# Kernel tuning notes

Measured on AMD Instinct MI355X. Metric: run time of the kernel, lower is better.

## Reference

```python
import jax, jax.numpy as jnp
import numpy as np

N_CH = 64
EPS = 1e-5


def _lhat():
    # adj=None branch: dist = ones - eye; adj_dist = exp(-dist/std) (torch.std is unbiased).
    dist = np.ones((N_CH, N_CH), np.float32) - np.eye(N_CH, dtype=np.float32)
    std = dist.std(ddof=1)
    A = np.exp(-dist / std).astype(np.float32)  # all entries > threshold=1e-4 -> fully connected w/ self loops
    deg = A.sum(axis=1)
    dinv = 1.0 / np.sqrt(deg)
    L = np.eye(N_CH, dtype=np.float32) - dinv[:, None] * A * dinv[None, :]  # sym-normalized Laplacian
    # ChebConv rescaling: Lhat = 2L/lambda_max - I with lambda_max=2 -> L - I
    return jnp.asarray(L - np.eye(N_CH, dtype=np.float32))


def _cheb(x, Lhat, W):
    # x: (B, N, Fin), W: (K, Fin, Fout). Chebyshev recursion, bias=False.
    Tx0 = x
    out = jnp.einsum('bnf,fo->bno', Tx0, W[0])
    Tx1 = jnp.einsum('nm,bmf->bnf', Lhat, Tx0)
    out = out + jnp.einsum('bnf,fo->bno', Tx1, W[1])
    for k in range(2, W.shape[0]):
        Tx2 = 2.0 * jnp.einsum('nm,bmf->bnf', Lhat, Tx1) - Tx0
        out = out + jnp.einsum('bnf,fo->bno', Tx2, W[k])
        Tx0, Tx1 = Tx1, Tx2
    return out


def _bn(x, g, b):
    # PyG BatchNorm (training mode): stats over all nodes in the batch -> axes (0,1).
    mu = jnp.mean(x, axis=(0, 1), keepdims=True)
    var = jnp.mean((x - mu) ** 2, axis=(0, 1), keepdims=True)
    return g * (x - mu) * jax.lax.rsqrt(var + EPS) + b


def setup_inputs() -> dict:
    key = jax.random.key(0)
    ks = jax.random.split(key, 4)
    B, F_IN, D = 4096, 256, 128
    x = jax.random.normal(ks[0], (B, N_CH, F_IN), dtype=jnp.float32)
    W1 = jax.random.normal(ks[1], (5, F_IN, D), dtype=jnp.float32) * 0.05
    W2 = jax.random.normal(ks[2], (3, D, D), dtype=jnp.float32) * 0.08
    W3 = jax.random.normal(ks[3], (3, D, D), dtype=jnp.float32) * 0.08
    ones = jnp.ones((D,), jnp.float32)
    zeros = jnp.zeros((D,), jnp.float32)
    return {'x': x, 'W1': W1, 'W2': W2, 'W3': W3,
            'g1': ones, 'b1': zeros, 'g2': ones, 'b2': zeros, 'g3': ones, 'b3': zeros}


def reference(x, W1, W2, W3, g1, b1, g2, b2, g3, b3):
    Lhat = _lhat()
    h = jax.nn.relu(_bn(_cheb(x, Lhat, W1), g1, b1))
    h = jax.nn.relu(_bn(_cheb(h, Lhat, W2), g2, b2))
    h = jax.nn.relu(_bn(_cheb(h, Lhat, W3), g3, b3))
    # global_mean_pool over nodes of each graph (dropout p=0 is identity)
    return jnp.mean(h, axis=1)  # (B, embed_dim)
```

## Files before the change

### kernel.cpp

```cpp
#include <hip/hip_runtime.h>
#include <cmath>


typedef __attribute__((ext_vector_type(8))) short bf16x8;
typedef __attribute__((ext_vector_type(4))) float f32x4;

typedef __attribute__((address_space(1))) const unsigned int guint_t;
typedef __attribute__((address_space(3))) unsigned int luint_t;

constexpr int BATCH = 4096;
constexpr int DCH   = 128;
constexpr float INV_NROWS = 1.0f / 262144.0f;

constexpr size_t OFF_G1   = 0;
constexpr size_t OFF_G2   = 32768;
constexpr size_t OFF_G3   = 49152;
constexpr size_t OFF_RAW  = 65536;
constexpr size_t OFF_Y    = 1180416;

struct Coeffs { float a[5]; float b[5]; };

__device__ __forceinline__ unsigned short f2bf(float f) {
  unsigned u = __float_as_uint(f);
  u += 0x7FFFu + ((u >> 16) & 1u);
  return (unsigned short)(u >> 16);
}
__device__ __forceinline__ float bf2f(unsigned short s) {
  return __uint_as_float(((unsigned)s) << 16);
}

__global__ __launch_bounds__(256) void prep_gran(const float* __restrict__ W1,
                                                 const float* __restrict__ W2,
                                                 const float* __restrict__ W3,
                                                 float* __restrict__ ws,
                                                 float* __restrict__ raw, Coeffs co)
{
  int id = blockIdx.x * 256 + threadIdx.x;
  if (id < 6144) raw[id] = 0.f;
  const float* W; int CIN, K, r; const float* cf; unsigned short* dst;
  if (id < 8192) {
    W = W1; CIN = 256; K = 5; r = id & 4095;
    cf = (id >= 4096) ? co.b : co.a;
    dst = (unsigned short*)(ws + OFF_G1) + (size_t)id * 8;
  } else if (id < 12288) {
    int e = id - 8192; W = W2; CIN = 128; K = 3; r = e & 2047;
    cf = (e >= 2048) ? co.b : co.a;
    dst = (unsigned short*)(ws + OFF_G2) + (size_t)e * 8;
  } else {
    int e = id - 12288; W = W3; CIN = 128; K = 3; r = e & 2047;
    cf = (e >= 2048) ? co.b : co.a;
    dst = (unsigned short*)(ws + OFF_G3) + (size_t)e * 8;
  }
  int kt  = r >> 9;
  int ct  = (r >> 6) & 7;
  int ln  = r & 63;
  int col = ct * 16 + (ln & 15);
  int f0  = kt * 32 + (ln >> 4) * 8;
  bf16x8 g;
#pragma unroll
  for (int i = 0; i < 8; ++i) {
    float s = 0.f;
    for (int k = 0; k < K; ++k)
      s = fmaf(cf[k], W[((size_t)k * CIN + f0 + i) * DCH + col], s);
    g[i] = (short)f2bf(s);
  }
  *reinterpret_cast<bf16x8*>(dst) = g;
}

template <int CIN, bool FIRST>
__global__ __launch_bounds__(512) void layer_k(
    const float* __restrict__ inF,
    const unsigned short* __restrict__ inB,
    unsigned short* __restrict__ yout,
    const unsigned short* __restrict__ gran,
    const float* __restrict__ rawIn,
    const float* __restrict__ gam, const float* __restrict__ bet,
    float* __restrict__ rawOut)
{
  constexpr int NKT = CIN / 32;
  constexpr int NG  = CIN * 16;

  __shared__ unsigned short sB[CIN * 256];
  __shared__ unsigned short slab[8][1152];
  __shared__ float sJw[4][2][DCH];
  __shared__ float sScale[DCH];
  __shared__ float sShift[DCH];

  const int tid = threadIdx.x;
  const int wv  = tid >> 6;
  const int p   = wv >> 1;
  const int h   = wv & 1;
  const int l   = tid & 63;
  const int lr  = l & 15;
  const int lk  = l >> 4;

  {
    const char* gB = reinterpret_cast<const char*>(gran);
    char* lB = reinterpret_cast<char*>(&sB[0]);
#pragma unroll
    for (int i = 0; i < (CIN * 512) / 8192; ++i) {
      const int c = i * 8 + wv;
      __builtin_amdgcn_global_load_lds(
          (guint_t*)(gB + (size_t)c * 1024 + (size_t)l * 16),
          (luint_t*)(lB + c * 1024), 16, 0, 0);
    }
  }
  if constexpr (!FIRST) {
    if (tid < DCH) {
      float ss = 0.f, qq = 0.f;
#pragma unroll
      for (int s = 0; s < 8; ++s) {
        ss += rawIn[s * 256 + tid];
        qq += rawIn[s * 256 + 128 + tid];
      }
      float mu  = ss * INV_NROWS;
      float var = qq * INV_NROWS - mu * mu;
      float rs  = rsqrtf(var + 1e-5f);
      float sc  = gam[tid] * rs;
      sScale[tid] = sc;
      sShift[tid] = fmaf(-mu, sc, bet[tid]);
    }
  }
  __syncthreads();

  const bf16x8* sBu = reinterpret_cast<const bf16x8*>(&sB[0]);

  float psum[8], psq[8];
#pragma unroll
  for (int ct = 0; ct < 8; ++ct) { psum[ct] = 0.f; psq[ct] = 0.f; }

#pragma unroll 1
  for (int it = 0; it < 4; ++it) {
    const int batch = blockIdx.x * 16 + it * 4 + p;

    f32x4 acc[8][2];
    f32x4 accJ[8];
#pragma unroll
    for (int ct = 0; ct < 8; ++ct) {
#pragma unroll
      for (int mt = 0; mt < 2; ++mt)
#pragma unroll
        for (int r = 0; r < 4; ++r) acc[ct][mt][r] = 0.f;
#pragma unroll
      for (int r = 0; r < 4; ++r) accJ[ct][r] = 0.f;
    }

#pragma unroll
    for (int kt = 0; kt < NKT; ++kt) {
      bf16x8 af[2];
      float vs[8];
#pragma unroll
      for (int i = 0; i < 8; ++i) vs[i] = 0.f;

      if constexpr (FIRST) {
        const float* ap = inF + ((size_t)batch * 64 + h * 32 + lr) * CIN + kt * 32 + lk * 8;
#pragma unroll
        for (int mt = 0; mt < 2; ++mt) {
          float4 u0 = *reinterpret_cast<const float4*>(ap + (size_t)mt * 16 * CIN);
          float4 u1 = *reinterpret_cast<const float4*>(ap + (size_t)mt * 16 * CIN + 4);
          float v8[8] = {u0.x, u0.y, u0.z, u0.w, u1.x, u1.y, u1.z, u1.w};
#pragma unroll
          for (int i = 0; i < 8; ++i) {
            vs[i] += v8[i];
            af[mt][i] = (short)f2bf(v8[i]);
          }
        }
      } else {
        const int c0 = kt * 32 + lk * 8;
        const float4 s0 = *reinterpret_cast<const float4*>(&sScale[c0]);
        const float4 s1 = *reinterpret_cast<const float4*>(&sScale[c0 + 4]);
        const float4 h0 = *reinterpret_cast<const float4*>(&sShift[c0]);
        const float4 h1 = *reinterpret_cast<const float4*>(&sShift[c0 + 4]);
        const float scv[8] = {s0.x, s0.y, s0.z, s0.w, s1.x, s1.y, s1.z, s1.w};
        const float shv[8] = {h0.x, h0.y, h0.z, h0.w, h1.x, h1.y, h1.z, h1.w};
        const bf16x8* yb = reinterpret_cast<const bf16x8*>(inB + (size_t)batch * 8192);
#pragma unroll
        for (int mt = 0; mt < 2; ++mt) {
          bf16x8 r16 = yb[kt * 256 + (h * 2 + mt) * 64 + l];
#pragma unroll
          for (int i = 0; i < 8; ++i) {
            float hv = fmaxf(fmaf(bf2f((unsigned short)r16[i]), scv[i], shv[i]), 0.f);
            vs[i] += hv;
            af[mt][i] = (short)f2bf(hv);
          }
        }
      }

      bf16x8 asum;
#pragma unroll
      for (int i = 0; i < 8; ++i) asum[i] = (short)f2bf(vs[i]);

      const bf16x8* bI = sBu + kt * 512 + l;
#pragma unroll
      for (int ct = 0; ct < 8; ++ct) {
        bf16x8 fI = bI[ct * 64];
        acc[ct][0] = __builtin_amdgcn_mfma_f32_16x16x32_bf16(af[0], fI, acc[ct][0], 0, 0, 0);
        acc[ct][1] = __builtin_amdgcn_mfma_f32_16x16x32_bf16(af[1], fI, acc[ct][1], 0, 0, 0);
      }
      const bf16x8* bJ = bI + NG;
#pragma unroll
      for (int ct = 0; ct < 8; ++ct)
        accJ[ct] = __builtin_amdgcn_mfma_f32_16x16x32_bf16(asum, bJ[ct * 64], accJ[ct], 0, 0, 0);
    }

#pragma unroll
    for (int ct = 0; ct < 8; ++ct) {
      float t = (accJ[ct][0] + accJ[ct][1]) + (accJ[ct][2] + accJ[ct][3]);
      t += __shfl_xor(t, 16);
      t += __shfl_xor(t, 32);
      if (lk == 0) sJw[p][h][ct * 16 + lr] = t;
    }
    __syncthreads();
    float jv[8];
#pragma unroll
    for (int ct = 0; ct < 8; ++ct)
      jv[ct] = sJw[p][0][ct * 16 + lr] + sJw[p][1][ct * 16 + lr];
    __syncthreads();

    unsigned short* myT = &slab[wv][0];
    bf16x8* yo = reinterpret_cast<bf16x8*>(yout + (size_t)batch * 8192);
#pragma unroll
    for (int mt = 0; mt < 2; ++mt) {
      const int m = h * 2 + mt;
#pragma unroll
      for (int cp = 0; cp < 2; ++cp) {
#pragma unroll
        for (int cq = 0; cq < 4; ++cq) {
          const int ct = cp * 4 + cq;
#pragma unroll
          for (int r = 0; r < 4; ++r) {
            float val = acc[ct][mt][r] + jv[ct];
            psum[ct] += val;
            psq[ct]  = fmaf(val, val, psq[ct]);
            myT[(lk * 4 + r) * 72 + cq * 16 + lr] = f2bf(val);
          }
        }
#pragma unroll
        for (int k2 = 0; k2 < 2; ++k2) {
          bf16x8 gd = *reinterpret_cast<const bf16x8*>(&myT[lr * 72 + k2 * 32 + lk * 8]);
          yo[(cp * 2 + k2) * 256 + m * 64 + l] = gd;
        }
      }
    }
  }

#pragma unroll
  for (int ct = 0; ct < 8; ++ct) {
    psum[ct] += __shfl_xor(psum[ct], 16);
    psum[ct] += __shfl_xor(psum[ct], 32);
    psq[ct]  += __shfl_xor(psq[ct], 16);
    psq[ct]  += __shfl_xor(psq[ct], 32);
  }
  if (lk == 0) {
    float* sRedW = reinterpret_cast<float*>(&slab[wv][0]);
#pragma unroll
    for (int ct = 0; ct < 8; ++ct) {
      sRedW[ct * 16 + lr]       = psum[ct];
      sRedW[128 + ct * 16 + lr] = psq[ct];
    }
  }
  __syncthreads();
  if (tid < 256) {
    const float* base = reinterpret_cast<const float*>(&slab[0][0]);
    float tot = 0.f;
#pragma unroll
    for (int w2 = 0; w2 < 8; ++w2) tot += base[w2 * 576 + tid];
    atomicAdd(&rawOut[(blockIdx.x & 7) * 256 + tid], tot);
  }
}

__global__ __launch_bounds__(256) void pool_k(const unsigned short* __restrict__ y,
                                              const float* __restrict__ raw3,
                                              const float* __restrict__ gam,
                                              const float* __restrict__ bet,
                                              float* __restrict__ out)
{
  __shared__ float sYp[64][132];
  __shared__ float sPool[2][DCH];
  __shared__ float sScale[DCH];
  __shared__ float sShift[DCH];
  const int b = blockIdx.x;
  const int t = threadIdx.x;
  const int wv = t >> 6, l = t & 63;
  const int row = wv * 16 + (l & 15);

  if (t < DCH) {
    float ss = 0.f, qq = 0.f;
#pragma unroll
    for (int s = 0; s < 8; ++s) {
      ss += raw3[s * 256 + t];
      qq += raw3[s * 256 + 128 + t];
    }
    float mu  = ss * INV_NROWS;
    float var = qq * INV_NROWS - mu * mu;
    float rr  = rsqrtf(var + 1e-5f);
    float sc  = gam[t] * rr;
    sScale[t] = sc;
    sShift[t] = fmaf(-mu, sc, bet[t]);
  }

#pragma unroll
  for (int kt = 0; kt < 4; ++kt) {
    bf16x8 r16 = *(reinterpret_cast<const bf16x8*>(y + (size_t)b * 8192) + (kt * 256 + t));
    const int feat = kt * 32 + (l >> 4) * 8;
    float4 f0, f1;
    f0.x = bf2f((unsigned short)r16[0]); f0.y = bf2f((unsigned short)r16[1]);
    f0.z = bf2f((unsigned short)r16[2]); f0.w = bf2f((unsigned short)r16[3]);
    f1.x = bf2f((unsigned short)r16[4]); f1.y = bf2f((unsigned short)r16[5]);
    f1.z = bf2f((unsigned short)r16[6]); f1.w = bf2f((unsigned short)r16[7]);
    *reinterpret_cast<float4*>(&sYp[row][feat])     = f0;
    *reinterpret_cast<float4*>(&sYp[row][feat + 4]) = f1;
  }
  __syncthreads();
  {
    const int c = t & 127, rg = t >> 7;
    float sc = sScale[c];
    float sh = sShift[c];
    float s = 0.f;
#pragma unroll 8
    for (int r = rg * 32; r < rg * 32 + 32; ++r)
      s += fmaxf(fmaf(sYp[r][c], sc, sh), 0.f);
    sPool[rg][c] = s;
  }
  __syncthreads();
  if (t < DCH)
    out[(size_t)b * DCH + t] = (sPool[0][t] + sPool[1][t]) * (1.0f / 64.0f);
}

extern "C" void kernel_launch(void* const* d_in, const int* in_sizes, int n_in,
                              void* d_out, int out_size, void* d_ws, size_t ws_size,
                              hipStream_t stream)
{
  const float* x  = (const float*)d_in[0];
  const float* W1 = (const float*)d_in[1];
  const float* W2 = (const float*)d_in[2];
  const float* W3 = (const float*)d_in[3];
  const float* g1 = (const float*)d_in[4];
  const float* b1 = (const float*)d_in[5];
  const float* g2 = (const float*)d_in[6];
  const float* b2 = (const float*)d_in[7];
  const float* g3 = (const float*)d_in[8];
  const float* b3 = (const float*)d_in[9];
  float* out = (float*)d_out;
  float* ws  = (float*)d_ws;

  Coeffs co;
  {
    double sd  = sqrt(63.0 / 4095.0);
    double av  = exp(-1.0 / sd);
    double deg = 1.0 + 63.0 * av;
    double al  = -(1.0 - av) / deg;
    double be  = -av / deg;
    double ak[5], bk[5];
    ak[0] = 1.0; bk[0] = 0.0;
    ak[1] = al;  bk[1] = be;
    for (int k = 2; k < 5; ++k) {
      ak[k] = 2.0 * al * ak[k - 1] - ak[k - 2];
      bk[k] = 2.0 * (be * ak[k - 1] + (al + 64.0 * be) * bk[k - 1]) - bk[k - 2];
    }
    for (int k = 0; k < 5; ++k) { co.a[k] = (float)ak[k]; co.b[k] = (float)bk[k]; }
  }

  const unsigned short* gr1 = (const unsigned short*)(ws + OFF_G1);
  const unsigned short* gr2 = (const unsigned short*)(ws + OFF_G2);
  const unsigned short* gr3 = (const unsigned short*)(ws + OFF_G3);
  float* raw1 = ws + OFF_RAW;
  float* raw2 = raw1 + 2048;
  float* raw3 = raw1 + 4096;
  unsigned short* yv = (unsigned short*)(ws + OFF_Y);

  prep_gran<<<64, 256, 0, stream>>>(W1, W2, W3, ws, raw1, co);

  layer_k<256, true ><<<256, 512, 0, stream>>>(x, nullptr, yv, gr1,
                                               nullptr, nullptr, nullptr, raw1);
  layer_k<128, false><<<256, 512, 0, stream>>>(nullptr, yv, yv, gr2,
                                               raw1, g1, b1, raw2);
  layer_k<128, false><<<256, 512, 0, stream>>>(nullptr, yv, yv, gr3,
                                               raw2, g2, b2, raw3);
  pool_k<<<BATCH, 256, 0, stream>>>(yv, raw3, g3, b3, out);

  (void)in_sizes; (void)n_in; (void)out_size; (void)ws_size;
}
```

Measured before the change: 185.9 us.

## Prefetch next batch inputs, double-buffer reductions, and simplify pooling to per-wave

The layer kernel now loads the next batch's input fragments into registers before the epilogue of the current batch. For the first layer only the first two K tiles are prefetched. The per-wave J-reduction buffer in shared memory is double-buffered, which removes one block barrier per iteration; a barrier is added before the final stats reduction reuses the slab. The pool kernel is rewritten so each wave handles one batch directly from registers with shuffle reductions, which removes the LDS staging and cuts the launch from 4096 to 1024 blocks. The cost is higher register pressure in the layer kernel, which could lower occupancy.

```diff
diff --git a/kernel.cpp b/kernel.cpp
--- a/kernel.cpp
+++ b/kernel.cpp
@@ -82,7 +82,7 @@
 
   __shared__ unsigned short sB[CIN * 256];
   __shared__ unsigned short slab[8][1152];
-  __shared__ float sJw[4][2][DCH];
+  __shared__ float sJw[2][4][2][DCH];
   __shared__ float sScale[DCH];
   __shared__ float sShift[DCH];
 
@@ -105,6 +105,31 @@
           (luint_t*)(lB + c * 1024), 16, 0, 0);
     }
   }
+
+  float4 pf[FIRST ? 8 : 1];
+  bf16x8 pb[FIRST ? 1 : 8];
+
+  {
+    const int b0 = blockIdx.x * 16 + p;
+    if constexpr (FIRST) {
+      const float* ap = inF + ((size_t)b0 * 64 + h * 32 + lr) * CIN + lk * 8;
+#pragma unroll
+      for (int kk = 0; kk < 2; ++kk)
+#pragma unroll
+        for (int mt = 0; mt < 2; ++mt) {
+          pf[kk * 4 + mt * 2 + 0] = *reinterpret_cast<const float4*>(ap + (size_t)mt * 16 * CIN + kk * 32);
+          pf[kk * 4 + mt * 2 + 1] = *reinterpret_cast<const float4*>(ap + (size_t)mt * 16 * CIN + kk * 32 + 4);
+        }
+    } else {
+      const bf16x8* yb0 = reinterpret_cast<const bf16x8*>(inB + (size_t)b0 * 8192);
+#pragma unroll
+      for (int kk = 0; kk < 4; ++kk)
+#pragma unroll
+        for (int mt = 0; mt < 2; ++mt)
+          pb[kk * 2 + mt] = yb0[kk * 256 + (h * 2 + mt) * 64 + l];
+    }
+  }
+
   if constexpr (!FIRST) {
     if (tid < DCH) {
       float ss = 0.f, qq = 0.f;
@@ -153,16 +178,30 @@
       for (int i = 0; i < 8; ++i) vs[i] = 0.f;
 
       if constexpr (FIRST) {
-        const float* ap = inF + ((size_t)batch * 64 + h * 32 + lr) * CIN + kt * 32 + lk * 8;
-#pragma unroll
-        for (int mt = 0; mt < 2; ++mt) {
-          float4 u0 = *reinterpret_cast<const float4*>(ap + (size_t)mt * 16 * CIN);
-          float4 u1 = *reinterpret_cast<const float4*>(ap + (size_t)mt * 16 * CIN + 4);
-          float v8[8] = {u0.x, u0.y, u0.z, u0.w, u1.x, u1.y, u1.z, u1.w};
-#pragma unroll
-          for (int i = 0; i < 8; ++i) {
-            vs[i] += v8[i];
-            af[mt][i] = (short)f2bf(v8[i]);
+        if (kt < 2) {
+#pragma unroll
+          for (int mt = 0; mt < 2; ++mt) {
+            float4 u0 = pf[kt * 4 + mt * 2 + 0];
+            float4 u1 = pf[kt * 4 + mt * 2 + 1];
+            float v8[8] = {u0.x, u0.y, u0.z, u0.w, u1.x, u1.y, u1.z, u1.w};
+#pragma unroll
+            for (int i = 0; i < 8; ++i) {
+              vs[i] += v8[i];
+              af[mt][i] = (short)f2bf(v8[i]);
+            }
+          }
+        } else {
+          const float* ap = inF + ((size_t)batch * 64 + h * 32 + lr) * CIN + kt * 32 + lk * 8;
+#pragma unroll
+          for (int mt = 0; mt < 2; ++mt) {
+            float4 u0 = *reinterpret_cast<const float4*>(ap + (size_t)mt * 16 * CIN);
+            float4 u1 = *reinterpret_cast<const float4*>(ap + (size_t)mt * 16 * CIN + 4);
+            float v8[8] = {u0.x, u0.y, u0.z, u0.w, u1.x, u1.y, u1.z, u1.w};
+#pragma unroll
+            for (int i = 0; i < 8; ++i) {
+              vs[i] += v8[i];
+              af[mt][i] = (short)f2bf(v8[i]);
+            }
           }
         }
       } else {
@@ -173,10 +212,9 @@
         const float4 h1 = *reinterpret_cast<const float4*>(&sShift[c0 + 4]);
         const float scv[8] = {s0.x, s0.y, s0.z, s0.w, s1.x, s1.y, s1.z, s1.w};
         const float shv[8] = {h0.x, h0.y, h0.z, h0.w, h1.x, h1.y, h1.z, h1.w};
-        const bf16x8* yb = reinterpret_cast<const bf16x8*>(inB + (size_t)batch * 8192);
 #pragma unroll
         for (int mt = 0; mt < 2; ++mt) {
-          bf16x8 r16 = yb[kt * 256 + (h * 2 + mt) * 64 + l];
+          bf16x8 r16 = pb[kt * 2 + mt];
 #pragma unroll
           for (int i = 0; i < 8; ++i) {
             float hv = fmaxf(fmaf(bf2f((unsigned short)r16[i]), scv[i], shv[i]), 0.f);
@@ -203,19 +241,39 @@
         accJ[ct] = __builtin_amdgcn_mfma_f32_16x16x32_bf16(asum, bJ[ct * 64], accJ[ct], 0, 0, 0);
     }
 
+    if (it + 1 < 4) {
+      const int nb = blockIdx.x * 16 + (it + 1) * 4 + p;
+      if constexpr (FIRST) {
+        const float* ap = inF + ((size_t)nb * 64 + h * 32 + lr) * CIN + lk * 8;
+#pragma unroll
+        for (int kk = 0; kk < 2; ++kk)
+#pragma unroll
+          for (int mt = 0; mt < 2; ++mt) {
+            pf[kk * 4 + mt * 2 + 0] = *reinterpret_cast<const float4*>(ap + (size_t)mt * 16 * CIN + kk * 32);
+            pf[kk * 4 + mt * 2 + 1] = *reinterpret_cast<const float4*>(ap + (size_t)mt * 16 * CIN + kk * 32 + 4);
+          }
+      } else {
+        const bf16x8* ybn = reinterpret_cast<const bf16x8*>(inB + (size_t)nb * 8192);
+#pragma unroll
+        for (int kk = 0; kk < 4; ++kk)
+#pragma unroll
+          for (int mt = 0; mt < 2; ++mt)
+            pb[kk * 2 + mt] = ybn[kk * 256 + (h * 2 + mt) * 64 + l];
+      }
+    }
+
 #pragma unroll
     for (int ct = 0; ct < 8; ++ct) {
       float t = (accJ[ct][0] + accJ[ct][1]) + (accJ[ct][2] + accJ[ct][3]);
       t += __shfl_xor(t, 16);
       t += __shfl_xor(t, 32);
-      if (lk == 0) sJw[p][h][ct * 16 + lr] = t;
+      if (lk == 0) sJw[it & 1][p][h][ct * 16 + lr] = t;
     }
     __syncthreads();
     float jv[8];
 #pragma unroll
     for (int ct = 0; ct < 8; ++ct)
-      jv[ct] = sJw[p][0][ct * 16 + lr] + sJw[p][1][ct * 16 + lr];
-    __syncthreads();
+      jv[ct] = sJw[it & 1][p][0][ct * 16 + lr] + sJw[it & 1][p][1][ct * 16 + lr];
 
     unsigned short* myT = &slab[wv][0];
     bf16x8* yo = reinterpret_cast<bf16x8*>(yout + (size_t)batch * 8192);
@@ -251,6 +309,7 @@
     psq[ct]  += __shfl_xor(psq[ct], 16);
     psq[ct]  += __shfl_xor(psq[ct], 32);
   }
+  __syncthreads();
   if (lk == 0) {
     float* sRedW = reinterpret_cast<float*>(&slab[wv][0]);
 #pragma unroll
@@ -275,14 +334,9 @@
                                               const float* __restrict__ bet,
                                               float* __restrict__ out)
 {
-  __shared__ float sYp[64][132];
-  __shared__ float sPool[2][DCH];
   __shared__ float sScale[DCH];
   __shared__ float sShift[DCH];
-  const int b = blockIdx.x;
   const int t = threadIdx.x;
-  const int wv = t >> 6, l = t & 63;
-  const int row = wv * 16 + (l & 15);
 
   if (t < DCH) {
     float ss = 0.f, qq = 0.f;
@@ -298,33 +352,46 @@
     sScale[t] = sc;
     sShift[t] = fmaf(-mu, sc, bet[t]);
   }
+  __syncthreads();
+
+  const int wv = t >> 6, l = t & 63;
+  const int lr = l & 15, lk = l >> 4;
+  const int batch = blockIdx.x * 4 + wv;
+  const bf16x8* yb = reinterpret_cast<const bf16x8*>(y + (size_t)batch * 8192);
 
 #pragma unroll
   for (int kt = 0; kt < 4; ++kt) {
-    bf16x8 r16 = *(reinterpret_cast<const bf16x8*>(y + (size_t)b * 8192) + (kt * 256 + t));
-    const int feat = kt * 32 + (l >> 4) * 8;
-    float4 f0, f1;
-    f0.x = bf2f((unsigned short)r16[0]); f0.y = bf2f((unsigned short)r16[1]);
-    f0.z = bf2f((unsigned short)r16[2]); f0.w = bf2f((unsigned short)r16[3]);
-    f1.x = bf2f((unsigned short)r16[4]); f1.y = bf2f((unsigned short)r16[5]);
-    f1.z = bf2f((unsigned short)r16[6]); f1.w = bf2f((unsigned short)r16[7]);
-    *reinterpret_cast<float4*>(&sYp[row][feat])     = f0;
-    *reinterpret_cast<float4*>(&sYp[row][feat + 4]) = f1;
-  }
-  __syncthreads();
-  {
-    const int c = t & 127, rg = t >> 7;
-    float sc = sScale[c];
-    float sh = sShift[c];
-    float s = 0.f;
-#pragma unroll 8
-    for (int r = rg * 32; r < rg * 32 + 32; ++r)
-      s += fmaxf(fmaf(sYp[r][c], sc, sh), 0.f);
-    sPool[rg][c] = s;
-  }
-  __syncthreads();
-  if (t < DCH)
-    out[(size_t)b * DCH + t] = (sPool[0][t] + sPool[1][t]) * (1.0f / 64.0f);
+    const int c0 = kt * 32 + lk * 8;
+    const float4 s0 = *reinterpret_cast<const float4*>(&sScale[c0]);
+    const float4 s1 = *reinterpret_cast<const float4*>(&sScale[c0 + 4]);
+    const float4 h0 = *reinterpret_cast<const float4*>(&sShift[c0]);
+    const float4 h1 = *reinterpret_cast<const float4*>(&sShift[c0 + 4]);
+    const float scv[8] = {s0.x, s0.y, s0.z, s0.w, s1.x, s1.y, s1.z, s1.w};
+    const float shv[8] = {h0.x, h0.y, h0.z, h0.w, h1.x, h1.y, h1.z, h1.w};
+    float s8[8];
+#pragma unroll
+    for (int i = 0; i < 8; ++i) s8[i] = 0.f;
+#pragma unroll
+    for (int m = 0; m < 4; ++m) {
+      bf16x8 g = yb[kt * 256 + m * 64 + l];
+#pragma unroll
+      for (int i = 0; i < 8; ++i)
+        s8[i] += fmaxf(fmaf(bf2f((unsigned short)g[i]), scv[i], shv[i]), 0.f);
+    }
+#pragma unroll
+    for (int mask = 1; mask <= 8; mask <<= 1)
+#pragma unroll
+      for (int i = 0; i < 8; ++i) s8[i] += __shfl_xor(s8[i], mask, 16);
+    if (lr == 0) {
+      float* op = out + (size_t)batch * DCH + c0;
+      *reinterpret_cast<float4*>(op) =
+          make_float4(s8[0] * (1.0f / 64.0f), s8[1] * (1.0f / 64.0f),
+                      s8[2] * (1.0f / 64.0f), s8[3] * (1.0f / 64.0f));
+      *reinterpret_cast<float4*>(op + 4) =
+          make_float4(s8[4] * (1.0f / 64.0f), s8[5] * (1.0f / 64.0f),
+                      s8[6] * (1.0f / 64.0f), s8[7] * (1.0f / 64.0f));
+    }
+  }
 }
 
 extern "C" void kernel_launch(void* const* d_in, const int* in_sizes, int n_in,
@@ -377,7 +444,7 @@
                                                raw1, g1, b1, raw2);
   layer_k<128, false><<<256, 512, 0, stream>>>(nullptr, yv, yv, gr3,
                                                raw2, g2, b2, raw3);
-  pool_k<<<BATCH, 256, 0, stream>>>(yv, raw3, g3, b3, out);
+  pool_k<<<1024, 256, 0, stream>>>(yv, raw3, g3, b3, out);
 
   (void)in_sizes; (void)n_in; (void)out_size; (void)ws_size;
 }
```

Result: faster. 170.6 us, median of 2 (-8.2%).
